# Optimization experiments

Hardware: AMD Instinct MI355X
Metric: run time of the kernel (lower is better)

Reference implementation:

```python
import jax, jax.numpy as jnp
import numpy as np

TOP_K = 5
TEMPERATURE = 0.1
EPS = 1e-12


def _normalize(x):
    # F.normalize(x, dim=-1): x / max(||x||, eps)
    n = jnp.linalg.norm(x, axis=-1, keepdims=True)
    return x / jnp.maximum(n, EPS)


def setup_inputs() -> dict:
    key = jax.random.key(0)
    k1, k2, k3 = jax.random.split(key, 3)
    B, N, D = 1024, 200000, 128
    query = jax.random.normal(k1, (B, D), dtype=jnp.float32)
    # memory bank stores L2-normalized keys (MemoryBank.build applies F.normalize)
    memory = _normalize(jax.random.normal(k2, (N, D), dtype=jnp.float32))
    index_map = jnp.arange(N, dtype=jnp.int64)
    exclude_indices = jax.random.randint(k3, (B,), 0, N, dtype=jnp.int64)
    return {"query": query, "memory": memory, "index_map": index_map,
            "exclude_indices": exclude_indices}


def reference(query, memory, index_map, exclude_indices):
    # cosine similarity: normalize query, memory is already normalized
    qn = _normalize(query)                       # [B, D]
    sim = qn @ memory.T                          # [B, N]
    # exclude own training sample (training-time self-exclusion)
    mask = exclude_indices[:, None] == index_map[None, :]   # [B, N]
    sim = jnp.where(mask, -jnp.inf, sim)
    # top-k (effective_top_k = min(top_k, N-1) = TOP_K here)
    top_sim, top_idx = jax.lax.top_k(sim, TOP_K)             # [B, K]
    weights = jax.nn.softmax(top_sim / TEMPERATURE, axis=-1)  # [B, K]
    vecs = memory[top_idx]                                   # [B, K, D]
    retrieved = jnp.einsum('bk,bkd->bd', weights, vecs)      # weighted sum
    retrieved = _normalize(retrieved)
    distances = 1.0 - top_sim[:, 0]                          # [B]
    return retrieved, distances, weights
```

## Files before the change

kernel.cpp:

```cpp
#include <hip/hip_runtime.h>
#include <math.h>

#define D128 128
#define TOPK 5
#define NP 200704
#define NCH2 12544
#define NSTRIP 392
#define MARGIN 0.008f
#define CAP 1024

typedef __attribute__((ext_vector_type(8))) short short8;
typedef __attribute__((ext_vector_type(4))) float f32x4;

__device__ __forceinline__ short f2bf(float f) {
    union { float f; unsigned u; } c; c.f = f;
    unsigned u = c.u + 0x7FFFu + ((c.u >> 16) & 1u);
    return (short)(u >> 16);
}

template <int NN>
__device__ __forceinline__ void insertg(float (&v)[NN], int (&x)[NN], float nv, int nj) {
    bool g[NN];
    #pragma unroll
    for (int i = 0; i < NN; ++i) g[i] = nv > v[i];
    #pragma unroll
    for (int i = NN - 1; i > 0; --i) {
        v[i] = g[i - 1] ? v[i - 1] : (g[i] ? nv : v[i]);
        x[i] = g[i - 1] ? x[i - 1] : (g[i] ? nj : x[i]);
    }
    v[0] = g[0] ? nv : v[0];
    x[0] = g[0] ? nj : x[0];
}
template <int NN>
__device__ __forceinline__ void insertv(float (&v)[NN], float nv) {
    bool g[NN];
    #pragma unroll
    for (int i = 0; i < NN; ++i) g[i] = nv > v[i];
    #pragma unroll
    for (int i = NN - 1; i > 0; --i)
        v[i] = g[i - 1] ? v[i - 1] : (g[i] ? nv : v[i]);
    v[0] = g[0] ? nv : v[0];
}

__global__ void qnorm_kernel(const float* __restrict__ q, float* __restrict__ qn,
                             short* __restrict__ qbf) {
    int b = blockIdx.x, t = threadIdx.x;
    float v0 = q[(size_t)b * D128 + t];
    float v1 = q[(size_t)b * D128 + t + 64];
    float ss = v0 * v0 + v1 * v1;
    #pragma unroll
    for (int off = 32; off > 0; off >>= 1) ss += __shfl_xor(ss, off, 64);
    float scale = 1.0f / fmaxf(sqrtf(ss), 1e-12f);
    float a0 = v0 * scale, a1 = v1 * scale;
    qn[(size_t)b * D128 + t] = a0;
    qn[(size_t)b * D128 + t + 64] = a1;
    qbf[(size_t)b * D128 + t] = f2bf(a0);
    qbf[(size_t)b * D128 + t + 64] = f2bf(a1);
}

__global__ void mconv_kernel(const float* __restrict__ mem, short* __restrict__ mbf, int N) {
    int idx = blockIdx.x * 256 + threadIdx.x;
    if (idx >= NP * 16) return;
    int row = idx >> 4, seg = idx & 15;
    short8 out;
    if (row < N) {
        const float* p = mem + (size_t)row * D128 + seg * 8;
        #pragma unroll
        for (int i = 0; i < 8; ++i) out[i] = f2bf(p[i]);
    } else {
        #pragma unroll
        for (int i = 0; i < 8; ++i) out[i] = 0;
    }
    *(short8*)(mbf + (size_t)row * D128 + seg * 8) = out;
}

#define MFMA16(a, b, c) __builtin_amdgcn_mfma_f32_16x16x32_bf16(a, b, c, 0, 0, 0)

__global__ __launch_bounds__(256, 3) void simtopk_max(
    const short* __restrict__ qbf, const short* __restrict__ mbf,
    _Float16* __restrict__ candT) {
    __shared__ short sK[64 * 136];
    __shared__ _Float16 sC[256 * 40];
    const int strip = blockIdx.x;
    const int qsg = blockIdx.y;
    const int t = threadIdx.x, w = t >> 6, lane = t & 63;
    const int n = lane & 15, quad = lane >> 4;
    const int qbase = qsg * 256 + w * 64;

    short8 bq[4][4];
    #pragma unroll
    for (int f = 0; f < 4; ++f) {
        const short* qrow = qbf + (size_t)(qbase + f * 16 + n) * D128 + quad * 8;
        #pragma unroll
        for (int s = 0; s < 4; ++s) bq[f][s] = *(const short8*)(qrow + s * 32);
    }

    const size_t k0 = (size_t)strip * 512;
    const int srow = t >> 4, scol = t & 15;
    const short* gbase = mbf + (k0 + srow) * D128 + scol * 8;

    short8 r0, r1, r2, r3;
    r0 = *(const short8*)(gbase + (size_t)0 * 16 * D128);
    r1 = *(const short8*)(gbase + (size_t)1 * 16 * D128);
    r2 = *(const short8*)(gbase + (size_t)2 * 16 * D128);
    r3 = *(const short8*)(gbase + (size_t)3 * 16 * D128);
    *(short8*)(&sK[(srow +  0) * 136 + scol * 8]) = r0;
    *(short8*)(&sK[(srow + 16) * 136 + scol * 8]) = r1;
    *(short8*)(&sK[(srow + 32) * 136 + scol * 8]) = r2;
    *(short8*)(&sK[(srow + 48) * 136 + scol * 8]) = r3;
    __syncthreads();
    {
        const short* g = gbase + (size_t)1 * 64 * D128;
        r0 = *(const short8*)(g + (size_t)0 * 16 * D128);
        r1 = *(const short8*)(g + (size_t)1 * 16 * D128);
        r2 = *(const short8*)(g + (size_t)2 * 16 * D128);
        r3 = *(const short8*)(g + (size_t)3 * 16 * D128);
    }

    for (int round = 0; round < 8; ++round) {
        #pragma unroll
        for (int tt = 0; tt < 4; ++tt) {
            const short* ab = &sK[(tt * 16 + n) * 136 + quad * 8];
            short8 a0 = *(const short8*)(ab);
            short8 a1 = *(const short8*)(ab + 32);
            short8 a2 = *(const short8*)(ab + 64);
            short8 a3 = *(const short8*)(ab + 96);
            f32x4 c0 = {0.f, 0.f, 0.f, 0.f}, c1 = c0, c2 = c0, c3 = c0;
            c0 = MFMA16(a0, bq[0][0], c0);
            c1 = MFMA16(a0, bq[1][0], c1);
            c2 = MFMA16(a0, bq[2][0], c2);
            c3 = MFMA16(a0, bq[3][0], c3);
            c0 = MFMA16(a1, bq[0][1], c0);
            c1 = MFMA16(a1, bq[1][1], c1);
            c2 = MFMA16(a1, bq[2][1], c2);
            c3 = MFMA16(a1, bq[3][1], c3);
            c0 = MFMA16(a2, bq[0][2], c0);
            c1 = MFMA16(a2, bq[1][2], c1);
            c2 = MFMA16(a2, bq[2][2], c2);
            c3 = MFMA16(a2, bq[3][2], c3);
            c0 = MFMA16(a3, bq[0][3], c0);
            c1 = MFMA16(a3, bq[1][3], c1);
            c2 = MFMA16(a3, bq[2][3], c2);
            c3 = MFMA16(a3, bq[3][3], c3);
            float m0 = fmaxf(fmaxf(c0[0], c0[1]), fmaxf(c0[2], c0[3]));
            float m1 = fmaxf(fmaxf(c1[0], c1[1]), fmaxf(c1[2], c1[3]));
            float m2 = fmaxf(fmaxf(c2[0], c2[1]), fmaxf(c2[2], c2[3]));
            float m3 = fmaxf(fmaxf(c3[0], c3[1]), fmaxf(c3[2], c3[3]));
            m0 = fmaxf(m0, __shfl_xor(m0, 16, 64)); m0 = fmaxf(m0, __shfl_xor(m0, 32, 64));
            m1 = fmaxf(m1, __shfl_xor(m1, 16, 64)); m1 = fmaxf(m1, __shfl_xor(m1, 32, 64));
            m2 = fmaxf(m2, __shfl_xor(m2, 16, 64)); m2 = fmaxf(m2, __shfl_xor(m2, 32, 64));
            m3 = fmaxf(m3, __shfl_xor(m3, 16, 64)); m3 = fmaxf(m3, __shfl_xor(m3, 32, 64));
            float msel = (quad == 0) ? m0 : (quad == 1) ? m1 : (quad == 2) ? m2 : m3;
            sC[(w * 64 + quad * 16 + n) * 40 + round * 4 + tt] = (_Float16)msel;
        }
        if (round < 7) {
            __syncthreads();
            *(short8*)(&sK[(srow +  0) * 136 + scol * 8]) = r0;
            *(short8*)(&sK[(srow + 16) * 136 + scol * 8]) = r1;
            *(short8*)(&sK[(srow + 32) * 136 + scol * 8]) = r2;
            *(short8*)(&sK[(srow + 48) * 136 + scol * 8]) = r3;
            __syncthreads();
            if (round < 6) {
                const short* g = gbase + (size_t)(round + 2) * 64 * D128;
                r0 = *(const short8*)(g + (size_t)0 * 16 * D128);
                r1 = *(const short8*)(g + (size_t)1 * 16 * D128);
                r2 = *(const short8*)(g + (size_t)2 * 16 * D128);
                r3 = *(const short8*)(g + (size_t)3 * 16 * D128);
            }
        }
    }

    __syncthreads();
    {
        int q = qsg * 256 + t;
        short* dst = (short*)candT + (size_t)q * NCH2 + strip * 32;
        #pragma unroll
        for (int j = 0; j < 4; ++j)
            *(short8*)(dst + j * 8) = *(const short8*)(&sC[t * 40 + j * 8]);
    }
}

__global__ __launch_bounds__(256, 4) void finalize_batch(
    const _Float16* __restrict__ candT, const float* __restrict__ mem,
    const float* __restrict__ qn, const int* __restrict__ index_map,
    const int* __restrict__ excl,
    float* __restrict__ outR, float* __restrict__ outD, float* __restrict__ outW, int N) {
    const int q = blockIdx.x, t = threadIdx.x;
    const int w = t >> 6, lane = t & 63;

    __shared__ _Float16 sM[NCH2];
    __shared__ float sQ[D128];
    __shared__ unsigned short sList[CAP];
    __shared__ int sCnt, sOv;
    __shared__ float sThr;
    __shared__ float sMrg[4 * 6];
    __shared__ float sWv[4 * TOPK];
    __shared__ int   sWk[4 * TOPK];
    __shared__ float sW[TOPK];
    __shared__ int   sJ[TOPK];

    if (t < 128) sQ[t] = qn[(size_t)q * D128 + t];
    if (t == 0) { sCnt = 0; sOv = 0; }
    {
        const short* crow = (const short*)candT + (size_t)q * NCH2;
        for (int i = t; i < NCH2 / 8; i += 256)
            *(short8*)(&sM[i * 8]) = *(const short8*)(crow + i * 8);
    }
    __syncthreads();

    float pv[6];
    #pragma unroll
    for (int i = 0; i < 6; ++i) pv[i] = -3e38f;
    for (int i = t; i < NCH2; i += 256) {
        float v = (float)sM[i];
        if (v > pv[5]) insertv<6>(pv, v);
    }
    #pragma unroll
    for (int r = 0; r < 6; ++r) {
        float bv = pv[0];
        #pragma unroll
        for (int off = 32; off > 0; off >>= 1) bv = fmaxf(bv, __shfl_xor(bv, off, 64));
        int ml = (pv[0] == bv) ? lane : 64;
        #pragma unroll
        for (int off = 32; off > 0; off >>= 1) ml = min(ml, __shfl_xor(ml, off, 64));
        if (lane == ml) {
            #pragma unroll
            for (int i = 0; i < 5; ++i) pv[i] = pv[i + 1];
            pv[5] = -3e38f;
        }
        if (lane == 0) sMrg[w * 6 + r] = bv;
    }
    __syncthreads();
    if (t == 0) {
        float b6[6];
        #pragma unroll
        for (int i = 0; i < 6; ++i) b6[i] = -3e38f;
        for (int j = 0; j < 24; ++j) {
            float v = sMrg[j];
            if (v > b6[5]) insertv<6>(b6, v);
        }
        sThr = b6[5] - 2.0f * MARGIN;
    }
    __syncthreads();

    const float thr = sThr;
    for (int i = t; i < NCH2; i += 256) {
        if ((float)sM[i] >= thr) {
            int p = atomicAdd(&sCnt, 1);
            if (p < CAP) sList[p] = (unsigned short)i; else sOv = 1;
        }
    }
    __syncthreads();
    const int ov = sOv;
    const int cnt = ov ? NCH2 : min(sCnt, CAP);

    const int exq = excl[q];
    float tv[TOPK]; int ti[TOPK];
    #pragma unroll
    for (int i = 0; i < TOPK; ++i) { tv[i] = -3e38f; ti[i] = -1; }
    const int rounds = (cnt + 15) >> 4;
    for (int r = 0; r < rounds; ++r) {
        int slot = r * 16 + (t >> 4);
        int ch = (slot < cnt) ? (ov ? slot : (int)sList[slot]) : -1;
        int key = ch * 16 + (t & 15);
        float v = -3e38f;
        if (ch >= 0 && key < N && index_map[key] != exq) {
            const float4* mr = (const float4*)(mem + (size_t)key * D128);
            const float4* qv = (const float4*)sQ;
            float acc = 0.f;
            #pragma unroll
            for (int d = 0; d < 32; ++d) {
                float4 a = mr[d], b = qv[d];
                acc += a.x * b.x + a.y * b.y + a.z * b.z + a.w * b.w;
            }
            v = acc;
        }
        if (v > tv[TOPK - 1]) insertg<TOPK>(tv, ti, v, key);
    }

    #pragma unroll
    for (int r = 0; r < TOPK; ++r) {
        float bv = tv[0]; int bk = ti[0];
        #pragma unroll
        for (int off = 32; off > 0; off >>= 1) {
            float ovv = __shfl_xor(bv, off, 64);
            int   okk = __shfl_xor(bk, off, 64);
            if (ovv > bv || (ovv == bv && (unsigned)okk < (unsigned)bk)) { bv = ovv; bk = okk; }
        }
        if (tv[0] == bv && ti[0] == bk) {
            #pragma unroll
            for (int i = 0; i < TOPK - 1; ++i) { tv[i] = tv[i + 1]; ti[i] = ti[i + 1]; }
            tv[TOPK - 1] = -3e38f; ti[TOPK - 1] = -1;
        }
        if (lane == 0) { sWv[w * TOPK + r] = bv; sWk[w * TOPK + r] = bk; }
    }
    __syncthreads();
    if (t == 0) {
        float bv[TOPK]; int bi[TOPK];
        #pragma unroll
        for (int i = 0; i < TOPK; ++i) { bv[i] = -3e38f; bi[i] = -1; }
        for (int j = 0; j < 4 * TOPK; ++j) {
            float v = sWv[j];
            if (v > bv[TOPK - 1]) insertg<TOPK>(bv, bi, v, sWk[j]);
        }
        float m = bv[0], ex[TOPK], sum = 0.f;
        #pragma unroll
        for (int k = 0; k < TOPK; ++k) { ex[k] = __expf((bv[k] - m) * 10.0f); sum += ex[k]; }
        float inv = 1.0f / sum;
        #pragma unroll
        for (int k = 0; k < TOPK; ++k) {
            float wk = ex[k] * inv;
            sW[k] = wk; sJ[k] = bi[k];
            outW[(size_t)q * TOPK + k] = wk;
        }
        outD[q] = 1.0f - bv[0];
    }
    __syncthreads();
    if (t < 64) {
        float r0 = 0.f, r1 = 0.f;
        #pragma unroll
        for (int k = 0; k < TOPK; ++k) {
            const float* mr = mem + (size_t)sJ[k] * D128;
            r0 += sW[k] * mr[t];
            r1 += sW[k] * mr[t + 64];
        }
        float ss = r0 * r0 + r1 * r1;
        #pragma unroll
        for (int off = 32; off > 0; off >>= 1) ss += __shfl_xor(ss, off, 64);
        float scale = 1.0f / fmaxf(sqrtf(ss), 1e-12f);
        outR[(size_t)q * D128 + t]      = r0 * scale;
        outR[(size_t)q * D128 + t + 64] = r1 * scale;
    }
}

extern "C" void kernel_launch(void* const* d_in, const int* in_sizes, int n_in,
                              void* d_out, int out_size, void* d_ws, size_t ws_size,
                              hipStream_t stream) {
    const float* query  = (const float*)d_in[0];
    const float* memory = (const float*)d_in[1];
    const int* index_map = (const int*)d_in[2];
    const int* excl      = (const int*)d_in[3];

    const int B = in_sizes[3];
    const int N = in_sizes[2];

    char* ws = (char*)d_ws;
    float*    qn    = (float*)(ws);
    short*    qbf   = (short*)(ws + 524288);
    short*    mbf   = (short*)(ws + 786432);
    _Float16* candT = (_Float16*)(ws + 52166656);

    float* outR = (float*)d_out;
    float* outD = outR + (size_t)B * D128;
    float* outW = outD + B;

    qnorm_kernel<<<B, 64, 0, stream>>>(query, qn, qbf);
    mconv_kernel<<<(NP * 16 + 255) / 256, 256, 0, stream>>>(memory, mbf, N);
    dim3 gridC(NSTRIP, 4);
    simtopk_max<<<gridC, 256, 0, stream>>>(qbf, mbf, candT);
    finalize_batch<<<B, 256, 0, stream>>>(candT, memory, qn, index_map, excl,
                                          outR, outD, outW, N);
}
```

Before: 282.9 us.

## Fuse bf16 memory conversion into similarity kernel and add per-strip max pruning

Drops the separate fp32-to-bf16 conversion kernel for the memory bank. The similarity kernel now loads fp32 rows directly and packs them to bf16 while staging into shared memory. The similarity kernel also writes a per-strip maximum. Finalize first thresholds the 392 strip maxima, then scans only the chunk maxima inside the surviving strips, instead of loading all 12544 chunk maxima per query. The fused kernel reads twice the bytes per tile and does the conversion once per query group, and the two-level filter adds an extra overflow path.

```diff
diff --git a/kernel.cpp b/kernel.cpp
--- a/kernel.cpp
+++ b/kernel.cpp
@@ -1,4 +1,5 @@
 #include <hip/hip_runtime.h>
+#include <hip/hip_bf16.h>
 #include <math.h>
 
 #define D128 128
@@ -8,6 +9,7 @@
 #define NSTRIP 392
 #define MARGIN 0.008f
 #define CAP 1024
+#define SCAP 96
 
 typedef __attribute__((ext_vector_type(8))) short short8;
 typedef __attribute__((ext_vector_type(4))) float f32x4;
@@ -16,6 +18,12 @@
     union { float f; unsigned u; } c; c.f = f;
     unsigned u = c.u + 0x7FFFu + ((c.u >> 16) & 1u);
     return (short)(u >> 16);
+}
+
+__device__ __forceinline__ unsigned pkbf(float x, float y) {
+    __hip_bfloat162 h = __float22bfloat162_rn(make_float2(x, y));
+    unsigned u; __builtin_memcpy(&u, &h, 4);
+    return u;
 }
 
 template <int NN>
@@ -58,27 +66,11 @@
     qbf[(size_t)b * D128 + t + 64] = f2bf(a1);
 }
 
-__global__ void mconv_kernel(const float* __restrict__ mem, short* __restrict__ mbf, int N) {
-    int idx = blockIdx.x * 256 + threadIdx.x;
-    if (idx >= NP * 16) return;
-    int row = idx >> 4, seg = idx & 15;
-    short8 out;
-    if (row < N) {
-        const float* p = mem + (size_t)row * D128 + seg * 8;
-        #pragma unroll
-        for (int i = 0; i < 8; ++i) out[i] = f2bf(p[i]);
-    } else {
-        #pragma unroll
-        for (int i = 0; i < 8; ++i) out[i] = 0;
-    }
-    *(short8*)(mbf + (size_t)row * D128 + seg * 8) = out;
-}
-
 #define MFMA16(a, b, c) __builtin_amdgcn_mfma_f32_16x16x32_bf16(a, b, c, 0, 0, 0)
 
 __global__ __launch_bounds__(256, 3) void simtopk_max(
-    const short* __restrict__ qbf, const short* __restrict__ mbf,
-    _Float16* __restrict__ candT) {
+    const short* __restrict__ qbf, const float* __restrict__ mem,
+    _Float16* __restrict__ candT, _Float16* __restrict__ stripT, int N) {
     __shared__ short sK[64 * 136];
     __shared__ _Float16 sC[256 * 40];
     const int strip = blockIdx.x;
@@ -97,25 +89,42 @@
 
     const size_t k0 = (size_t)strip * 512;
     const int srow = t >> 4, scol = t & 15;
-    const short* gbase = mbf + (k0 + srow) * D128 + scol * 8;
-
-    short8 r0, r1, r2, r3;
-    r0 = *(const short8*)(gbase + (size_t)0 * 16 * D128);
-    r1 = *(const short8*)(gbase + (size_t)1 * 16 * D128);
-    r2 = *(const short8*)(gbase + (size_t)2 * 16 * D128);
-    r3 = *(const short8*)(gbase + (size_t)3 * 16 * D128);
-    *(short8*)(&sK[(srow +  0) * 136 + scol * 8]) = r0;
-    *(short8*)(&sK[(srow + 16) * 136 + scol * 8]) = r1;
-    *(short8*)(&sK[(srow + 32) * 136 + scol * 8]) = r2;
-    *(short8*)(&sK[(srow + 48) * 136 + scol * 8]) = r3;
-    __syncthreads();
-    {
-        const short* g = gbase + (size_t)1 * 64 * D128;
-        r0 = *(const short8*)(g + (size_t)0 * 16 * D128);
-        r1 = *(const short8*)(g + (size_t)1 * 16 * D128);
-        r2 = *(const short8*)(g + (size_t)2 * 16 * D128);
-        r3 = *(const short8*)(g + (size_t)3 * 16 * D128);
-    }
+    const float* gbase = mem + (k0 + srow) * (size_t)D128 + scol * 8;
+    const bool tail = (k0 + 512 > (size_t)N);
+
+    float4 fa[8];
+
+    auto loadg = [&](int g) {
+        const float* base = gbase + (size_t)g * 64 * D128;
+        #pragma unroll
+        for (int i = 0; i < 4; ++i) {
+            const float4* p = (const float4*)(base + (size_t)i * 16 * D128);
+            if (tail) {
+                size_t key = k0 + (size_t)(g * 64 + srow + i * 16);
+                if (key >= (size_t)N) p = (const float4*)mem;
+            }
+            fa[2 * i]     = p[0];
+            fa[2 * i + 1] = p[1];
+        }
+    };
+    auto storesk = [&](int g) {
+        #pragma unroll
+        for (int i = 0; i < 4; ++i) {
+            uint4 wv;
+            wv.x = pkbf(fa[2 * i].x,     fa[2 * i].y);
+            wv.y = pkbf(fa[2 * i].z,     fa[2 * i].w);
+            wv.z = pkbf(fa[2 * i + 1].x, fa[2 * i + 1].y);
+            wv.w = pkbf(fa[2 * i + 1].z, fa[2 * i + 1].w);
+            if (tail && (k0 + (size_t)(g * 64 + srow + i * 16) >= (size_t)N))
+                wv = make_uint4(0, 0, 0, 0);
+            *((uint4*)&sK[(srow + 16 * i) * 136 + scol * 8]) = wv;
+        }
+    };
+
+    loadg(0);
+    storesk(0);
+    __syncthreads();
+    loadg(1);
 
     for (int round = 0; round < 8; ++round) {
         #pragma unroll
@@ -155,18 +164,9 @@
         }
         if (round < 7) {
             __syncthreads();
-            *(short8*)(&sK[(srow +  0) * 136 + scol * 8]) = r0;
-            *(short8*)(&sK[(srow + 16) * 136 + scol * 8]) = r1;
-            *(short8*)(&sK[(srow + 32) * 136 + scol * 8]) = r2;
-            *(short8*)(&sK[(srow + 48) * 136 + scol * 8]) = r3;
+            storesk(round + 1);
             __syncthreads();
-            if (round < 6) {
-                const short* g = gbase + (size_t)(round + 2) * 64 * D128;
-                r0 = *(const short8*)(g + (size_t)0 * 16 * D128);
-                r1 = *(const short8*)(g + (size_t)1 * 16 * D128);
-                r2 = *(const short8*)(g + (size_t)2 * 16 * D128);
-                r3 = *(const short8*)(g + (size_t)3 * 16 * D128);
-            }
+            if (round < 6) loadg(round + 2);
         }
     }
 
@@ -174,24 +174,34 @@
     {
         int q = qsg * 256 + t;
         short* dst = (short*)candT + (size_t)q * NCH2 + strip * 32;
-        #pragma unroll
-        for (int j = 0; j < 4; ++j)
-            *(short8*)(dst + j * 8) = *(const short8*)(&sC[t * 40 + j * 8]);
+        float mx = -3e38f;
+        #pragma unroll
+        for (int j = 0; j < 4; ++j) {
+            short8 v = *(const short8*)(&sC[t * 40 + j * 8]);
+            *(short8*)(dst + j * 8) = v;
+            #pragma unroll
+            for (int e = 0; e < 8; ++e) {
+                short sv = v[e]; _Float16 hv; __builtin_memcpy(&hv, &sv, 2);
+                mx = fmaxf(mx, (float)hv);
+            }
+        }
+        stripT[(size_t)q * NSTRIP + strip] = (_Float16)mx;
     }
 }
 
 __global__ __launch_bounds__(256, 4) void finalize_batch(
-    const _Float16* __restrict__ candT, const float* __restrict__ mem,
-    const float* __restrict__ qn, const int* __restrict__ index_map,
-    const int* __restrict__ excl,
+    const _Float16* __restrict__ candT, const _Float16* __restrict__ stripT,
+    const float* __restrict__ mem, const float* __restrict__ qn,
+    const int* __restrict__ index_map, const int* __restrict__ excl,
     float* __restrict__ outR, float* __restrict__ outD, float* __restrict__ outW, int N) {
     const int q = blockIdx.x, t = threadIdx.x;
     const int w = t >> 6, lane = t & 63;
 
-    __shared__ _Float16 sM[NCH2];
-    __shared__ float sQ[D128];
+    __shared__ __align__(16) float sQ[D128];
+    __shared__ __align__(16) _Float16 sS[NSTRIP];
+    __shared__ unsigned short sStr[SCAP];
     __shared__ unsigned short sList[CAP];
-    __shared__ int sCnt, sOv;
+    __shared__ int sScnt, sSov, sCnt, sOv;
     __shared__ float sThr;
     __shared__ float sMrg[4 * 6];
     __shared__ float sWv[4 * TOPK];
@@ -200,19 +210,17 @@
     __shared__ int   sJ[TOPK];
 
     if (t < 128) sQ[t] = qn[(size_t)q * D128 + t];
-    if (t == 0) { sCnt = 0; sOv = 0; }
-    {
-        const short* crow = (const short*)candT + (size_t)q * NCH2;
-        for (int i = t; i < NCH2 / 8; i += 256)
-            *(short8*)(&sM[i * 8]) = *(const short8*)(crow + i * 8);
-    }
+    if (t == 0) { sScnt = 0; sSov = 0; sCnt = 0; sOv = 0; }
+    if (t < NSTRIP / 8)
+        *(short8*)(&sS[t * 8]) =
+            *(const short8*)((const short*)stripT + (size_t)q * NSTRIP + t * 8);
     __syncthreads();
 
     float pv[6];
     #pragma unroll
     for (int i = 0; i < 6; ++i) pv[i] = -3e38f;
-    for (int i = t; i < NCH2; i += 256) {
-        float v = (float)sM[i];
+    for (int i = t; i < NSTRIP; i += 256) {
+        float v = (float)sS[i];
         if (v > pv[5]) insertv<6>(pv, v);
     }
     #pragma unroll
@@ -244,14 +252,30 @@
     __syncthreads();
 
     const float thr = sThr;
-    for (int i = t; i < NCH2; i += 256) {
-        if ((float)sM[i] >= thr) {
-            int p = atomicAdd(&sCnt, 1);
-            if (p < CAP) sList[p] = (unsigned short)i; else sOv = 1;
-        }
-    }
-    __syncthreads();
-    const int ov = sOv;
+    for (int i = t; i < NSTRIP; i += 256) {
+        if ((float)sS[i] >= thr) {
+            int p = atomicAdd(&sScnt, 1);
+            if (p < SCAP) sStr[p] = (unsigned short)i; else sSov = 1;
+        }
+    }
+    __syncthreads();
+    const int scnt = min(sScnt, SCAP);
+
+    if (!sSov) {
+        for (int base = 0; base < scnt; base += 8) {
+            int si = base + (t >> 5);
+            if (si < scnt) {
+                int ch = (int)sStr[si] * 32 + (t & 31);
+                float v = (float)candT[(size_t)q * NCH2 + ch];
+                if (v >= thr) {
+                    int p = atomicAdd(&sCnt, 1);
+                    if (p < CAP) sList[p] = (unsigned short)ch; else sOv = 1;
+                }
+            }
+        }
+    }
+    __syncthreads();
+    const int ov = (sSov || sOv) ? 1 : 0;
     const int cnt = ov ? NCH2 : min(sCnt, CAP);
 
     const int exq = excl[q];
@@ -345,19 +369,18 @@
     const int N = in_sizes[2];
 
     char* ws = (char*)d_ws;
-    float*    qn    = (float*)(ws);
-    short*    qbf   = (short*)(ws + 524288);
-    short*    mbf   = (short*)(ws + 786432);
-    _Float16* candT = (_Float16*)(ws + 52166656);
+    float*    qn     = (float*)(ws);
+    short*    qbf    = (short*)(ws + 524288);
+    _Float16* candT  = (_Float16*)(ws + 786432);
+    _Float16* stripT = (_Float16*)(ws + 786432 + 25690112);
 
     float* outR = (float*)d_out;
     float* outD = outR + (size_t)B * D128;
     float* outW = outD + B;
 
     qnorm_kernel<<<B, 64, 0, stream>>>(query, qn, qbf);
-    mconv_kernel<<<(NP * 16 + 255) / 256, 256, 0, stream>>>(memory, mbf, N);
     dim3 gridC(NSTRIP, 4);
-    simtopk_max<<<gridC, 256, 0, stream>>>(qbf, mbf, candT);
-    finalize_batch<<<B, 256, 0, stream>>>(candT, memory, qn, index_map, excl,
+    simtopk_max<<<gridC, 256, 0, stream>>>(qbf, memory, candT, stripT, N);
+    finalize_batch<<<B, 256, 0, stream>>>(candT, stripT, memory, qn, index_map, excl,
                                           outR, outD, outW, N);
 }
```

After: 259.6 us. -8.2%, faster.
